# Performance work log

Measured on AMD Instinct MI355X. Metric: run time of the kernel, lower is better.

## Reference

```python
import jax, jax.numpy as jnp
import numpy as np

N_ENT, N_REL, N_TRIG, N_ARGS = 100000, 250000, 50000, 250000
ENT_DIM, REL_R, RTYPE_DIM, ROLE_DIM, REL_SIZE = 288, 256, 32, 256, 200
ARG_DIM = REL_R + RTYPE_DIM + ENT_DIM  # 576


def setup_inputs() -> dict:
    key = jax.random.key(0)
    ks = jax.random.split(key, 11)
    s_in = 1.0 / np.sqrt(ARG_DIM)
    return {
        "ent_embeds": jax.random.normal(ks[0], (N_ENT, ENT_DIM), jnp.float32),
        "rel_embeds": jax.random.normal(ks[1], (N_REL, REL_R), jnp.float32),
        "rtype_table": jax.random.normal(ks[2], (REL_SIZE + 1, RTYPE_DIM), jnp.float32),
        "W_in": jax.random.normal(ks[3], (ARG_DIM, ROLE_DIM), jnp.float32) * s_in,
        "W_out": jax.random.normal(ks[4], (ARG_DIM, ROLE_DIM), jnp.float32) * s_in,
        "rtype_ids": jax.random.randint(ks[5], (N_REL,), 0, REL_SIZE, jnp.int32),
        "trig_ent_id": jax.random.randint(ks[6], (N_TRIG,), 0, N_ENT, jnp.int32),
        "arg_trig": jax.random.randint(ks[7], (N_ARGS,), 0, N_TRIG, jnp.int32),
        "arg_rel": jax.random.randint(ks[8], (N_ARGS,), 0, N_REL, jnp.int32),
        "arg_ent": jax.random.randint(ks[9], (N_ARGS,), 0, N_ENT, jnp.int32),
        "arg_is_in": jax.random.randint(ks[10], (N_ARGS,), 0, 2, jnp.int32),
    }


def reference(ent_embeds, rel_embeds, rtype_table, W_in, W_out,
              rtype_ids, trig_ent_id, arg_trig, arg_rel, arg_ent, arg_is_in):
    # per-relation type embedding (rtype_embedding_layer)
    rt_embeds = rtype_table[rtype_ids]                       # [N_REL, RTYPE_DIM]
    # per-argument gather + concat (get_arg_embeds): [rel | rtype | arg-entity]
    x = jnp.concatenate([rel_embeds[arg_rel],
                         rt_embeds[arg_rel],
                         ent_embeds[arg_ent]], axis=-1)      # [N_ARGS, ARG_DIM]
    # in_arg_layer vs out_arg_layer selected per argument (io_ids membership)
    m = arg_is_in.astype(x.dtype)[:, None]
    y = (x * m) @ W_in + (x * (1.0 - m)) @ W_out             # [N_ARGS, ROLE_DIM]
    # sum-aggregate per trigger (torch.sum over stacked arg embeds)
    args_sum = jax.ops.segment_sum(y, arg_trig, num_segments=N_TRIG)
    # concat trigger embedding with aggregated args (event_representation)
    return jnp.concatenate([ent_embeds[trig_ent_id], args_sum], axis=-1)  # [N_TRIG, ENT_DIM+ROLE_DIM]
```

## Files before the change

kernel.cpp:

```cpp
#include <hip/hip_runtime.h>
#include <hip/hip_bf16.h>
#include <stdint.h>

#define N_ENT    100000
#define N_REL    250000
#define N_TRIG   50000
#define N_ARGS   250000
#define ENT_DIM  288
#define REL_R    256
#define RTYPE_DIM 32
#define ROLE_DIM 256
#define ARG_DIM  576
#define OUT_DIM  544

#define BM 64
#define BK 32
#define NSTEP (ARG_DIM / BK)
#define LDP 40

typedef __attribute__((ext_vector_type(8))) short bf16x8;
typedef __attribute__((ext_vector_type(4))) short bf16x4;
typedef __attribute__((ext_vector_type(4))) float f32x4;

__device__ __forceinline__ short f2b(float f) {
    union { float f; uint32_t u; } v; v.f = f;
    uint32_t u = v.u;
    uint32_t r = (u + 0x7fffu + ((u >> 16) & 1u)) >> 16;
    return (short)r;
}

__global__ void __launch_bounds__(256)
k_init(const float* __restrict__ ent, const int* __restrict__ trig_ent,
       float* __restrict__ out)
{
    const int t    = blockIdx.x * 4 + (threadIdx.x >> 6);
    const int lane = threadIdx.x & 63;
    const int e    = trig_ent[t];
    const float4* src = (const float4*)(ent + (size_t)e * ENT_DIM);
    float4*       dst = (float4*)(out + (size_t)t * OUT_DIM);
    const float4 z = {0.f, 0.f, 0.f, 0.f};
    dst[lane] = src[lane];
    if (lane < 8) dst[64 + lane] = src[64 + lane];
    dst[72 + lane] = z;
}

__global__ void __launch_bounds__(256)
k_prep(const float* __restrict__ W_in, const float* __restrict__ W_out,
       short* __restrict__ Wb)
{
    const int idx = blockIdx.x * 256 + threadIdx.x;
    const int w   = idx / (ARG_DIM * ROLE_DIM);
    const int rem = idx % (ARG_DIM * ROLE_DIM);
    const int k   = rem / ROLE_DIM;
    const int col = rem % ROLE_DIM;
    const float* src = (w == 0) ? W_in : W_out;
    Wb[((size_t)w * ROLE_DIM + col) * ARG_DIM + k] = f2b(src[k * ROLE_DIM + col]);
}

__global__ void __launch_bounds__(512, 4)
k_gemm(const float* __restrict__ ent,  const float* __restrict__ rel,
       const float* __restrict__ rtab, const short* __restrict__ Wb,
       const int* __restrict__ rtype_ids, const int* __restrict__ arg_trig,
       const int* __restrict__ arg_rel,   const int* __restrict__ arg_ent,
       const int* __restrict__ arg_is_in, float* __restrict__ out)
{
    __shared__ short As[2][BM][LDP];
    __shared__ int s_rel[BM], s_ent[BM], s_rt[BM], s_trig[BM], s_mask[BM];

    const int tid = threadIdx.x;
    const int a0  = blockIdx.x * BM;

    if (tid < BM) {
        int a     = a0 + tid;
        int valid = (a < N_ARGS);
        int aa    = valid ? a : (N_ARGS - 1);
        int r     = arg_rel[aa];
        s_rel[tid]  = r;
        s_ent[tid]  = arg_ent[aa];
        s_rt[tid]   = rtype_ids[r];
        s_trig[tid] = arg_trig[aa];
        s_mask[tid] = valid ? arg_is_in[aa] : -1;
    }
    __syncthreads();

    const int lane  = tid & 63;
    const int wave  = tid >> 6;
    const int quad  = lane >> 4;
    const int l15   = lane & 15;
    const int nbase = wave * 32;

    const int srow = tid >> 3;
    const int skq  = (tid & 7) * 4;

    const float* p_rel = rel  + (size_t)s_rel[srow] * REL_R    + skq;
    const float* p_rt  = rtab + s_rt[srow] * RTYPE_DIM         + skq;
    const float* p_ent = ent  + (size_t)s_ent[srow] * ENT_DIM  + skq;

    const short* wbl = Wb + (size_t)(nbase + l15) * ARG_DIM + quad * 8;

    int rowmask[4];
#pragma unroll
    for (int m = 0; m < 4; ++m) rowmask[m] = s_mask[m * 16 + l15];

    f32x4 acc[4][2];
#pragma unroll
    for (int m = 0; m < 4; ++m)
#pragma unroll
        for (int n = 0; n < 2; ++n) acc[m][n] = (f32x4){0.f, 0.f, 0.f, 0.f};

    const bf16x8 zf = {0, 0, 0, 0, 0, 0, 0, 0};

    float4 vA = *(const float4*)(p_rel);
    float4 vB = *(const float4*)(p_rel + BK);
    float4 vC = *(const float4*)(p_rel + 2 * BK);

    auto STEP = [&](int s, float4& w) {
        bf16x4 h;
        h[0] = f2b(w.x); h[1] = f2b(w.y); h[2] = f2b(w.z); h[3] = f2b(w.w);
        *(bf16x4*)&As[s & 1][srow][skq] = h;

        asm volatile("s_waitcnt lgkmcnt(0)" ::: "memory");
        __builtin_amdgcn_s_barrier();
        asm volatile("" ::: "memory");

        bf16x8 a[4];
#pragma unroll
        for (int m = 0; m < 4; ++m)
            a[m] = *(const bf16x8*)&As[s & 1][m * 16 + l15][quad * 8];

        const short* bp = wbl + s * BK;
        const bf16x8 bi0 = *(const bf16x8*)(bp);
        const bf16x8 bi1 = *(const bf16x8*)(bp + 16 * ARG_DIM);
        const bf16x8 bo0 = *(const bf16x8*)(bp + (size_t)ROLE_DIM * ARG_DIM);
        const bf16x8 bo1 = *(const bf16x8*)(bp + (size_t)(ROLE_DIM + 16) * ARG_DIM);

#pragma unroll
        for (int m = 0; m < 4; ++m) {
            const bf16x8 ain = (rowmask[m] == 1) ? a[m] : zf;
            const bf16x8 aot = (rowmask[m] == 0) ? a[m] : zf;
            acc[m][0] = __builtin_amdgcn_mfma_f32_16x16x32_bf16(ain, bi0, acc[m][0], 0, 0, 0);
            acc[m][0] = __builtin_amdgcn_mfma_f32_16x16x32_bf16(aot, bo0, acc[m][0], 0, 0, 0);
            acc[m][1] = __builtin_amdgcn_mfma_f32_16x16x32_bf16(ain, bi1, acc[m][1], 0, 0, 0);
            acc[m][1] = __builtin_amdgcn_mfma_f32_16x16x32_bf16(aot, bo1, acc[m][1], 0, 0, 0);
        }

        __builtin_amdgcn_sched_barrier(0);
        if (s + 3 < NSTEP) {
            const int sn = s + 3;
            const float* src = (sn < 8)  ? (p_rel + sn * BK)
                             : (sn == 8) ? p_rt
                                         : (p_ent + (sn - 9) * BK);
            w = *(const float4*)src;
        }
    };

#pragma unroll
    for (int ss = 0; ss < NSTEP; ss += 3) {
        STEP(ss,     vA);
        STEP(ss + 1, vB);
        STEP(ss + 2, vC);
    }

#pragma unroll
    for (int m = 0; m < 4; ++m) {
#pragma unroll
        for (int r4 = 0; r4 < 4; ++r4) {
            const int row = m * 16 + quad * 4 + r4;
            if (s_mask[row] < 0) continue;
            float* dst = out + (size_t)s_trig[row] * OUT_DIM + ENT_DIM
                             + nbase + l15;
            atomicAdd(dst,      acc[m][0][r4]);
            atomicAdd(dst + 16, acc[m][1][r4]);
        }
    }
}

extern "C" void kernel_launch(void* const* d_in, const int* in_sizes, int n_in,
                              void* d_out, int out_size, void* d_ws, size_t ws_size,
                              hipStream_t stream)
{
    const float* ent      = (const float*)d_in[0];
    const float* rel      = (const float*)d_in[1];
    const float* rtab     = (const float*)d_in[2];
    const float* W_in     = (const float*)d_in[3];
    const float* W_out    = (const float*)d_in[4];
    const int*  rtype_ids = (const int*)d_in[5];
    const int*  trig_ent  = (const int*)d_in[6];
    const int*  arg_trig  = (const int*)d_in[7];
    const int*  arg_rel   = (const int*)d_in[8];
    const int*  arg_ent   = (const int*)d_in[9];
    const int*  arg_is_in = (const int*)d_in[10];

    float* out = (float*)d_out;
    short* Wb  = (short*)d_ws;

    hipLaunchKernelGGL(k_init, dim3(N_TRIG / 4), dim3(256), 0, stream,
                       ent, trig_ent, out);
    hipLaunchKernelGGL(k_prep, dim3(2 * ARG_DIM * ROLE_DIM / 256), dim3(256), 0,
                       stream, W_in, W_out, Wb);
    hipLaunchKernelGGL(k_gemm, dim3((N_ARGS + BM - 1) / BM), dim3(512), 0, stream,
                       ent, rel, rtab, Wb,
                       rtype_ids, arg_trig, arg_rel, arg_ent, arg_is_in, out);
}
```

Before: 832.4 us.

## Counting-sort arguments by trigger and segment-reduce in LDS before atomics

After: 801.5 us. 3.7% less time.

```diff
diff --git a/kernel.cpp b/kernel.cpp
--- a/kernel.cpp
+++ b/kernel.cpp
@@ -17,6 +17,7 @@
 #define BK 32
 #define NSTEP (ARG_DIM / BK)
 #define LDP 40
+#define CSP 258
 
 typedef __attribute__((ext_vector_type(8))) short bf16x8;
 typedef __attribute__((ext_vector_type(4))) short bf16x4;
@@ -57,29 +58,90 @@
     Wb[((size_t)w * ROLE_DIM + col) * ARG_DIM + k] = f2b(src[k * ROLE_DIM + col]);
 }
 
+__global__ void __launch_bounds__(256)
+k_hist(const int* __restrict__ arg_trig, int* __restrict__ cnt)
+{
+    const int a = blockIdx.x * 256 + threadIdx.x;
+    if (a < N_ARGS) atomicAdd(&cnt[arg_trig[a]], 1);
+}
+
+#define SCAN_T 1024
+#define SCAN_B ((N_TRIG + SCAN_T - 1) / SCAN_T)
+
+__global__ void __launch_bounds__(SCAN_T)
+k_scan1(const int* __restrict__ cnt, int* __restrict__ off,
+        int* __restrict__ bsum)
+{
+    __shared__ int buf[SCAN_T];
+    const int tid = threadIdx.x;
+    const int i   = blockIdx.x * SCAN_T + tid;
+    int v = (i < N_TRIG) ? cnt[i] : 0;
+    buf[tid] = v;
+    __syncthreads();
+#pragma unroll
+    for (int o = 1; o < SCAN_T; o <<= 1) {
+        int x = (tid >= o) ? buf[tid - o] : 0;
+        __syncthreads();
+        buf[tid] += x;
+        __syncthreads();
+    }
+    if (i < N_TRIG) off[i] = buf[tid] - v;
+    if (tid == SCAN_T - 1) bsum[blockIdx.x] = buf[tid];
+}
+
+__global__ void __launch_bounds__(64)
+k_scan2(int* __restrict__ bsum)
+{
+    if (threadIdx.x == 0) {
+        int s = 0;
+        for (int i = 0; i < SCAN_B; ++i) { int t = bsum[i]; bsum[i] = s; s += t; }
+    }
+}
+
+__global__ void __launch_bounds__(SCAN_T)
+k_scan3(int* __restrict__ off, const int* __restrict__ bsum)
+{
+    const int i = blockIdx.x * SCAN_T + threadIdx.x;
+    if (i < N_TRIG) off[i] += bsum[blockIdx.x];
+}
+
+__global__ void __launch_bounds__(256)
+k_scatter(const int* __restrict__ arg_trig, const int* __restrict__ off,
+          int* __restrict__ cur, int* __restrict__ idx)
+{
+    const int a = blockIdx.x * 256 + threadIdx.x;
+    if (a < N_ARGS) {
+        const int t = arg_trig[a];
+        const int p = atomicAdd(&cur[t], 1);
+        idx[off[t] + p] = a;
+    }
+}
+
 __global__ void __launch_bounds__(512, 4)
 k_gemm(const float* __restrict__ ent,  const float* __restrict__ rel,
        const float* __restrict__ rtab, const short* __restrict__ Wb,
        const int* __restrict__ rtype_ids, const int* __restrict__ arg_trig,
        const int* __restrict__ arg_rel,   const int* __restrict__ arg_ent,
-       const int* __restrict__ arg_is_in, float* __restrict__ out)
+       const int* __restrict__ arg_is_in, const int* __restrict__ idx,
+       float* __restrict__ out)
 {
     __shared__ short As[2][BM][LDP];
+    __shared__ float Cs[BM][CSP];
     __shared__ int s_rel[BM], s_ent[BM], s_rt[BM], s_trig[BM], s_mask[BM];
 
     const int tid = threadIdx.x;
     const int a0  = blockIdx.x * BM;
 
     if (tid < BM) {
-        int a     = a0 + tid;
-        int valid = (a < N_ARGS);
-        int aa    = valid ? a : (N_ARGS - 1);
-        int r     = arg_rel[aa];
+        int i     = a0 + tid;
+        int valid = (i < N_ARGS);
+        int a     = idx[valid ? i : (N_ARGS - 1)];
+        int r     = arg_rel[a];
         s_rel[tid]  = r;
-        s_ent[tid]  = arg_ent[aa];
+        s_ent[tid]  = arg_ent[a];
         s_rt[tid]   = rtype_ids[r];
-        s_trig[tid] = arg_trig[aa];
-        s_mask[tid] = valid ? arg_is_in[aa] : -1;
+        s_trig[tid] = valid ? arg_trig[a] : -1;
+        s_mask[tid] = valid ? arg_is_in[a] : -1;
     }
     __syncthreads();
 
@@ -162,15 +224,38 @@
     }
 
 #pragma unroll
-    for (int m = 0; m < 4; ++m) {
-#pragma unroll
-        for (int r4 = 0; r4 < 4; ++r4) {
-            const int row = m * 16 + quad * 4 + r4;
-            if (s_mask[row] < 0) continue;
-            float* dst = out + (size_t)s_trig[row] * OUT_DIM + ENT_DIM
-                             + nbase + l15;
-            atomicAdd(dst,      acc[m][0][r4]);
-            atomicAdd(dst + 16, acc[m][1][r4]);
+    for (int m = 0; m < 4; ++m)
+#pragma unroll
+        for (int n = 0; n < 2; ++n)
+#pragma unroll
+            for (int r4 = 0; r4 < 4; ++r4)
+                Cs[m * 16 + quad * 4 + r4][nbase + n * 16 + l15] = acc[m][n][r4];
+    __syncthreads();
+
+    {
+        const int c    = tid & 255;
+        const int half = tid >> 8;
+        const int r0   = half * 32;
+        const int rend = r0 + 32;
+
+        int   runTrig  = s_trig[r0];
+        int   runStart = r0;
+        float sum      = 0.f;
+        for (int r = r0; r < rend; ++r) {
+            const int t = s_trig[r];
+            if (t != runTrig) {
+                if (runTrig >= 0) {
+                    float* p = out + (size_t)runTrig * OUT_DIM + ENT_DIM + c;
+                    if (runStart == r0) atomicAdd(p, sum);
+                    else                *p = sum;
+                }
+                runTrig = t; runStart = r; sum = 0.f;
+            }
+            sum += Cs[r][c];
+        }
+        if (runTrig >= 0) {
+            float* p = out + (size_t)runTrig * OUT_DIM + ENT_DIM + c;
+            atomicAdd(p, sum);
         }
     }
 }
@@ -192,13 +277,31 @@
     const int*  arg_is_in = (const int*)d_in[10];
 
     float* out = (float*)d_out;
-    short* Wb  = (short*)d_ws;
+
+    char* ws   = (char*)d_ws;
+    short* Wb  = (short*)(ws);
+    int*   cnt = (int*)(ws + 589824);
+    int*   cur = (int*)(ws + 789824);
+    int*   off = (int*)(ws + 989824);
+    int*   bsum= (int*)(ws + 1190080);
+    int*   idx = (int*)(ws + 1190400);
+
+    hipMemsetAsync(cnt, 0, 400000, stream);
 
     hipLaunchKernelGGL(k_init, dim3(N_TRIG / 4), dim3(256), 0, stream,
                        ent, trig_ent, out);
     hipLaunchKernelGGL(k_prep, dim3(2 * ARG_DIM * ROLE_DIM / 256), dim3(256), 0,
                        stream, W_in, W_out, Wb);
+    hipLaunchKernelGGL(k_hist, dim3((N_ARGS + 255) / 256), dim3(256), 0, stream,
+                       arg_trig, cnt);
+    hipLaunchKernelGGL(k_scan1, dim3(SCAN_B), dim3(SCAN_T), 0, stream,
+                       cnt, off, bsum);
+    hipLaunchKernelGGL(k_scan2, dim3(1), dim3(64), 0, stream, bsum);
+    hipLaunchKernelGGL(k_scan3, dim3(SCAN_B), dim3(SCAN_T), 0, stream,
+                       off, bsum);
+    hipLaunchKernelGGL(k_scatter, dim3((N_ARGS + 255) / 256), dim3(256), 0,
+                       stream, arg_trig, off, cur, idx);
     hipLaunchKernelGGL(k_gemm, dim3((N_ARGS + BM - 1) / BM), dim3(512), 0, stream,
                        ent, rel, rtab, Wb,
-                       rtype_ids, arg_trig, arg_rel, arg_ent, arg_is_in, out);
-}
+                       rtype_ids, arg_trig, arg_rel, arg_ent, arg_is_in, idx, out);
+}
```
